# Performance work log

Hardware: AMD Instinct MI355X
Metric: run time of the kernel (lower is better)

## Reference

```python
import jax, jax.numpy as jnp
import numpy as np

B, H, S, D = 2, 16, 2048, 64
SOFTCLAMP = 50.0


def setup_inputs() -> dict:
    key = jax.random.key(0)
    kq, kk, kv, km = jax.random.split(key, 4)
    q = jax.random.normal(kq, (B, H, S, D), dtype=jnp.float32)
    k = jax.random.normal(kk, (B, H, S, D), dtype=jnp.float32)
    v = jax.random.normal(kv, (B, H, S, D), dtype=jnp.float32)
    mask = jax.random.randint(km, (B, S), 0, 2).astype(jnp.bool_)
    return {"q": q, "k": k, "v": v, "mask": mask}


def reference(q, k, v, mask):
    scale = q.shape[-1] ** -0.5
    # [b, h, i, j] similarity logits
    sim = jnp.einsum('bhid,bhjd->bhij', q, k) * scale
    # tanh-based logit softclamping (Gemma2-style softcapping)
    sim = jnp.tanh(sim / SOFTCLAMP) * SOFTCLAMP
    mask_value = -jnp.finfo(sim.dtype).max
    sim = jnp.where(mask[:, None, None, :], sim, mask_value)
    attn = jax.nn.softmax(sim, axis=-1)
    out = jnp.einsum('bhij,bhjd->bhid', attn, v)
    return out, attn
```

## Files before the change

kernel.cpp:

```cpp
#include <hip/hip_runtime.h>
#include <hip/hip_bf16.h>

#define B_ 2
#define H_ 16
#define S_ 2048
#define D_ 64
#define BUFSTR 72
#define BUFSZ (16 * BUFSTR)

typedef float f32x4 __attribute__((ext_vector_type(4)));
typedef short s16x8 __attribute__((ext_vector_type(8)));
typedef short s16x4 __attribute__((ext_vector_type(4)));

__device__ __forceinline__ short f2bf(float f) {
  unsigned u = __float_as_uint(f);
  u += 0x7FFFu + ((u >> 16) & 1u);
  return (short)(u >> 16);
}
__device__ __forceinline__ float bf2f(short s) {
  return __uint_as_float(((unsigned)(unsigned short)s) << 16);
}
__device__ __forceinline__ unsigned cvt_pk_bf16(float lo, float hi) {
  unsigned r;
  asm("v_cvt_pk_bf16_f32 %0, %1, %2" : "=v"(r) : "v"(lo), "v"(hi));
  return r;
}

__device__ __forceinline__ float softcap_p(float a) {
  const float k1 = 0.18033688011f;
  const float k2 = -3.7570183e-07f;
  const float k3 = 9.3926761e-13f;
  const float C  = 72.134752044f;
  float y = a * a;
  float t = __builtin_fmaf(y, k3, k2);
  t = __builtin_fmaf(y, t, k1);
  float arg = __builtin_fmaf(a, t, -C);
  arg = fminf(arg, 0.f);
  return exp2f(arg);
}

__global__ __launch_bounds__(256) void prep_qk(const float* __restrict__ q,
                                               const float* __restrict__ k,
                                               short* __restrict__ qbf,
                                               short* __restrict__ kbf) {
  size_t i = ((size_t)blockIdx.x * 256 + threadIdx.x) * 8;
  const f32x4* qa = (const f32x4*)(q + i);
  const f32x4* ka = (const f32x4*)(k + i);
  f32x4 a0 = __builtin_nontemporal_load(qa);
  f32x4 a1 = __builtin_nontemporal_load(qa + 1);
  f32x4 b0 = __builtin_nontemporal_load(ka);
  f32x4 b1 = __builtin_nontemporal_load(ka + 1);
  s16x8 oq, ok;
  #pragma unroll
  for (int e = 0; e < 4; ++e) {
    oq[e] = f2bf(a0[e]); oq[4 + e] = f2bf(a1[e]);
    ok[e] = f2bf(b0[e]); ok[4 + e] = f2bf(b1[e]);
  }
  *(s16x8*)(qbf + i) = oq;
  *(s16x8*)(kbf + i) = ok;
}

__global__ __launch_bounds__(256) void prep_v(const float* __restrict__ v,
                                              short* __restrict__ vt) {
  __shared__ float tile[64][65];
  const int tid = threadIdx.x;
  const int j0 = blockIdx.x * 64;
  const int bh = blockIdx.y;
  const float* vh = v + (size_t)bh * S_ * D_;
  #pragma unroll
  for (int it = 0; it < 16; ++it) {
    int idx = it * 256 + tid;
    int row = idx >> 6, col = idx & 63;
    tile[row][col] = __builtin_nontemporal_load(&vh[(size_t)(j0 + row) * D_ + col]);
  }
  __syncthreads();
  short* vth = vt + (size_t)bh * D_ * S_;
  #pragma unroll
  for (int it = 0; it < 16; ++it) {
    int idx = it * 256 + tid;
    int d = idx >> 6, jj = idx & 63;
    vth[(size_t)d * S_ + j0 + jj] = f2bf(tile[jj][d]);
  }
}

template <bool PRE>
__global__ __launch_bounds__(512, 2) void attend_fused(
    const float* __restrict__ q, const float* __restrict__ k,
    const float* __restrict__ v, const int* __restrict__ mask,
    const short* __restrict__ qbf, const short* __restrict__ kbf,
    const short* __restrict__ vt,
    float* __restrict__ out, float* __restrict__ attn) {
  __shared__ float pvred[8][16][64];
  __shared__ float ls_rs[8][16];
  __shared__ float ls_rinv[16];

  const int tid  = threadIdx.x;
  const int wv   = tid >> 6;
  const int lane = tid & 63;
  const int lg   = lane >> 4;
  const int li   = lane & 15;

  const unsigned flat = blockIdx.y * gridDim.x + blockIdx.x;
  const unsigned swz  = (flat & 7) * 512 + (flat >> 3);
  const int q0 = (int)(swz & 127) * 16;
  const int bh = (int)(swz >> 7);
  const int b  = bh >> 4;
  const int* mrow = mask + (size_t)b * S_;

  short* myb = (short*)pvred + wv * BUFSZ;

  s16x8 qf0, qf1;
  if constexpr (PRE) {
    const short* qr = qbf + ((size_t)bh * S_ + q0 + li) * D_ + lg * 8;
    qf0 = *(const s16x8*)qr;
    qf1 = *(const s16x8*)(qr + 32);
  } else {
    const float* qr = q + ((size_t)bh * S_ + q0 + li) * D_ + lg * 8;
    #pragma unroll
    for (int e = 0; e < 8; ++e) { qf0[e] = f2bf(qr[e]); qf1[e] = f2bf(qr[32 + e]); }
  }

  float rs[4] = {0.f, 0.f, 0.f, 0.f};
  f32x4 pvacc[4];
  #pragma unroll
  for (int m = 0; m < 4; ++m) pvacc[m] = (f32x4){0.f, 0.f, 0.f, 0.f};
  unsigned st[4][4][2];

  #pragma unroll
  for (int c = 0; c < 4; ++c) {
    const int jc = c * 512 + wv * 64;

    f32x4 acc[4];
    #pragma unroll
    for (int n = 0; n < 4; ++n) acc[n] = (f32x4){0.f, 0.f, 0.f, 0.f};
    #pragma unroll
    for (int n = 0; n < 4; ++n) {
      if constexpr (PRE) {
        const short* kr = kbf + ((size_t)bh * S_ + jc + n * 16 + li) * D_ + lg * 8;
        acc[n] = __builtin_amdgcn_mfma_f32_16x16x32_bf16(qf0, *(const s16x8*)kr, acc[n], 0, 0, 0);
        acc[n] = __builtin_amdgcn_mfma_f32_16x16x32_bf16(qf1, *(const s16x8*)(kr + 32), acc[n], 0, 0, 0);
      } else {
        const float* kr = k + ((size_t)bh * S_ + jc + n * 16 + li) * D_ + lg * 8;
        s16x8 k0, k1;
        #pragma unroll
        for (int e = 0; e < 8; ++e) { k0[e] = f2bf(kr[e]); k1[e] = f2bf(kr[32 + e]); }
        acc[n] = __builtin_amdgcn_mfma_f32_16x16x32_bf16(qf0, k0, acc[n], 0, 0, 0);
        acc[n] = __builtin_amdgcn_mfma_f32_16x16x32_bf16(qf1, k1, acc[n], 0, 0, 0);
      }
    }

    #pragma unroll
    for (int n = 0; n < 4; ++n) {
      const bool keep = mrow[jc + n * 16 + li] != 0;
      float p[4];
      #pragma unroll
      for (int r = 0; r < 4; ++r) {
        float pp = softcap_p(acc[n][r]);
        p[r] = keep ? pp : 0.f;
        rs[r] += p[r];
      }
      unsigned pk0 = cvt_pk_bf16(p[0], p[1]);
      unsigned pk1 = cvt_pk_bf16(p[2], p[3]);
      st[c][n][0] = pk0;
      st[c][n][1] = pk1;
      const int col = n * 16 + li;
      myb[(lg * 4 + 0) * BUFSTR + col] = (short)(pk0 & 0xFFFFu);
      myb[(lg * 4 + 1) * BUFSTR + col] = (short)(pk0 >> 16);
      myb[(lg * 4 + 2) * BUFSTR + col] = (short)(pk1 & 0xFFFFu);
      myb[(lg * 4 + 3) * BUFSTR + col] = (short)(pk1 >> 16);
    }

    #pragma unroll
    for (int ks = 0; ks < 2; ++ks) {
      s16x8 pa = *(const s16x8*)&myb[li * BUFSTR + ks * 32 + lg * 8];
      #pragma unroll
      for (int m = 0; m < 4; ++m) {
        s16x8 vb;
        if constexpr (PRE) {
          vb = *(const s16x8*)(vt + ((size_t)bh * D_ + m * 16 + li) * S_ + jc + ks * 32 + lg * 8);
        } else {
          const float* vp = v + (size_t)bh * S_ * D_ + (size_t)(jc + ks * 32 + lg * 8) * D_ + m * 16 + li;
          #pragma unroll
          for (int e = 0; e < 8; ++e) vb[e] = f2bf(vp[(size_t)e * D_]);
        }
        pvacc[m] = __builtin_amdgcn_mfma_f32_16x16x32_bf16(pa, vb, pvacc[m], 0, 0, 0);
      }
    }
  }

  #pragma unroll
  for (int r = 0; r < 4; ++r) {
    #pragma unroll
    for (int m = 1; m < 16; m <<= 1) rs[r] += __shfl_xor(rs[r], m, 64);
  }
  if (li == 0) {
    #pragma unroll
    for (int r = 0; r < 4; ++r) ls_rs[wv][lg * 4 + r] = rs[r];
  }
  __syncthreads();
  if (tid < 16) {
    float ssum = 0.f;
    #pragma unroll
    for (int w = 0; w < 8; ++w) ssum += ls_rs[w][tid];
    ls_rinv[tid] = (ssum > 0.f) ? 1.f / ssum : 0.f;
  }
  __syncthreads();

  const int rrow = lane >> 3;
  const int rseg = lane & 7;
  const float rv0 = ls_rinv[rrow];
  const float rv1 = ls_rinv[8 + rrow];
  float* abase = attn + ((size_t)bh * S_ + q0) * S_;

  #pragma unroll
  for (int c = 0; c < 4; ++c) {
    const int jc = c * 512 + wv * 64;
    #pragma unroll
    for (int n = 0; n < 4; ++n) {
      const int col = n * 16 + li;
      #pragma unroll
      for (int rr = 0; rr < 2; ++rr) {
        unsigned pk = st[c][n][rr];
        myb[(lg * 4 + 2 * rr) * BUFSTR + col] = (short)(pk & 0xFFFFu);
        myb[(lg * 4 + 2 * rr + 1) * BUFSTR + col] = (short)(pk >> 16);
      }
    }
    #pragma unroll
    for (int half = 0; half < 2; ++half) {
      const int row = half * 8 + rrow;
      const float rv = half ? rv1 : rv0;
      #pragma unroll
      for (int jh = 0; jh < 2; ++jh) {
        s16x4 pb = *(const s16x4*)&myb[row * BUFSTR + jh * 32 + rseg * 4];
        f32x4 a;
        a[0] = bf2f(pb[0]) * rv; a[1] = bf2f(pb[1]) * rv;
        a[2] = bf2f(pb[2]) * rv; a[3] = bf2f(pb[3]) * rv;
        __builtin_nontemporal_store(a, (f32x4*)(abase + (size_t)row * S_ + jc + jh * 32 + rseg * 4));
      }
    }
  }

  __syncthreads();

  #pragma unroll
  for (int m = 0; m < 4; ++m)
    #pragma unroll
    for (int r = 0; r < 4; ++r)
      pvred[wv][lg * 4 + r][m * 16 + li] = pvacc[m][r];
  __syncthreads();

  #pragma unroll
  for (int h = 0; h < 2; ++h) {
    const int idx = h * 512 + tid;
    const int qq = idx >> 6, d = idx & 63;
    float ssum = 0.f;
    #pragma unroll
    for (int w = 0; w < 8; ++w) ssum += pvred[w][qq][d];
    out[((size_t)bh * S_ + q0 + qq) * D_ + d] = ssum * ls_rinv[qq];
  }
}

extern "C" void kernel_launch(void* const* d_in, const int* in_sizes, int n_in,
                              void* d_out, int out_size, void* d_ws, size_t ws_size,
                              hipStream_t stream) {
  const float* q = (const float*)d_in[0];
  const float* k = (const float*)d_in[1];
  const float* v = (const float*)d_in[2];
  const int* mask = (const int*)d_in[3];

  float* out  = (float*)d_out;
  const size_t nel = (size_t)B_ * H_ * S_ * D_;
  float* attn = out + nel;

  dim3 grid(S_ / 16, B_ * H_);
  const size_t need = nel * 2 * 3;

  if (ws_size >= need) {
    short* qbf = (short*)d_ws;
    short* kbf = qbf + nel;
    short* vtp = kbf + nel;
    prep_qk<<<(int)(nel / (256 * 8)), 256, 0, stream>>>(q, k, qbf, kbf);
    prep_v<<<dim3(S_ / 64, B_ * H_), 256, 0, stream>>>(v, vtp);
    attend_fused<true><<<grid, 512, 0, stream>>>(q, k, v, mask, qbf, kbf, vtp, out, attn);
  } else {
    attend_fused<false><<<grid, 512, 0, stream>>>(q, k, v, mask, nullptr, nullptr, nullptr, out, attn);
  }
}
```

Measured before the change: 317.8 us.

## Keep full probability strip in LDS and prefetch next K chunk

Replaces the per-wave 16x72 bf16 scratch buffer and register-held packed probabilities with a shared 16x2056 bf16 strip covering the whole key range. Each wave then writes two complete attention rows with contiguous 1 KB-per-iteration stores instead of 64-column fragments. The QK^T K fragments are also software-prefetched one chunk ahead into registers. This raises LDS use to about 66 KB per block, which may limit the two-blocks-per-CU occupancy target, and it adds more scalar LDS stores in place of the packed conversion.

```diff
diff --git a/kernel.cpp b/kernel.cpp
--- a/kernel.cpp
+++ b/kernel.cpp
@@ -5,8 +5,7 @@
 #define H_ 16
 #define S_ 2048
 #define D_ 64
-#define BUFSTR 72
-#define BUFSZ (16 * BUFSTR)
+#define PSTR 2056
 
 typedef float f32x4 __attribute__((ext_vector_type(4)));
 typedef short s16x8 __attribute__((ext_vector_type(8)));
@@ -19,11 +18,6 @@
 }
 __device__ __forceinline__ float bf2f(short s) {
   return __uint_as_float(((unsigned)(unsigned short)s) << 16);
-}
-__device__ __forceinline__ unsigned cvt_pk_bf16(float lo, float hi) {
-  unsigned r;
-  asm("v_cvt_pk_bf16_f32 %0, %1, %2" : "=v"(r) : "v"(lo), "v"(hi));
-  return r;
 }
 
 __device__ __forceinline__ float softcap_p(float a) {
@@ -90,7 +84,7 @@
     const short* __restrict__ qbf, const short* __restrict__ kbf,
     const short* __restrict__ vt,
     float* __restrict__ out, float* __restrict__ attn) {
-  __shared__ float pvred[8][16][64];
+  __shared__ short strip[16 * PSTR];
   __shared__ float ls_rs[8][16];
   __shared__ float ls_rinv[16];
 
@@ -106,8 +100,6 @@
   const int bh = (int)(swz >> 7);
   const int b  = bh >> 4;
   const int* mrow = mask + (size_t)b * S_;
-
-  short* myb = (short*)pvred + wv * BUFSZ;
 
   s16x8 qf0, qf1;
   if constexpr (PRE) {
@@ -120,11 +112,24 @@
     for (int e = 0; e < 8; ++e) { qf0[e] = f2bf(qr[e]); qf1[e] = f2bf(qr[32 + e]); }
   }
 
+  const short* kbase = PRE ? (kbf + (size_t)bh * S_ * D_) : nullptr;
+  s16x8 kf[8];
+
+  auto ldK = [&](int cc) {
+    const int jcc = cc * 512 + wv * 64;
+    #pragma unroll
+    for (int n = 0; n < 4; ++n) {
+      const short* kr = kbase + (size_t)(jcc + n * 16 + li) * D_ + lg * 8;
+      kf[2 * n]     = *(const s16x8*)kr;
+      kf[2 * n + 1] = *(const s16x8*)(kr + 32);
+    }
+  };
+  if constexpr (PRE) ldK(0);
+
   float rs[4] = {0.f, 0.f, 0.f, 0.f};
   f32x4 pvacc[4];
   #pragma unroll
   for (int m = 0; m < 4; ++m) pvacc[m] = (f32x4){0.f, 0.f, 0.f, 0.f};
-  unsigned st[4][4][2];
 
   #pragma unroll
   for (int c = 0; c < 4; ++c) {
@@ -133,13 +138,16 @@
     f32x4 acc[4];
     #pragma unroll
     for (int n = 0; n < 4; ++n) acc[n] = (f32x4){0.f, 0.f, 0.f, 0.f};
-    #pragma unroll
-    for (int n = 0; n < 4; ++n) {
-      if constexpr (PRE) {
-        const short* kr = kbf + ((size_t)bh * S_ + jc + n * 16 + li) * D_ + lg * 8;
-        acc[n] = __builtin_amdgcn_mfma_f32_16x16x32_bf16(qf0, *(const s16x8*)kr, acc[n], 0, 0, 0);
-        acc[n] = __builtin_amdgcn_mfma_f32_16x16x32_bf16(qf1, *(const s16x8*)(kr + 32), acc[n], 0, 0, 0);
-      } else {
+    if constexpr (PRE) {
+      #pragma unroll
+      for (int n = 0; n < 4; ++n) {
+        acc[n] = __builtin_amdgcn_mfma_f32_16x16x32_bf16(qf0, kf[2 * n], acc[n], 0, 0, 0);
+        acc[n] = __builtin_amdgcn_mfma_f32_16x16x32_bf16(qf1, kf[2 * n + 1], acc[n], 0, 0, 0);
+      }
+      if (c < 3) ldK(c + 1);
+    } else {
+      #pragma unroll
+      for (int n = 0; n < 4; ++n) {
         const float* kr = k + ((size_t)bh * S_ + jc + n * 16 + li) * D_ + lg * 8;
         s16x8 k0, k1;
         #pragma unroll
@@ -151,28 +159,20 @@
 
     #pragma unroll
     for (int n = 0; n < 4; ++n) {
-      const bool keep = mrow[jc + n * 16 + li] != 0;
-      float p[4];
+      const int j = jc + n * 16 + li;
+      const bool keep = mrow[j] != 0;
       #pragma unroll
       for (int r = 0; r < 4; ++r) {
         float pp = softcap_p(acc[n][r]);
-        p[r] = keep ? pp : 0.f;
-        rs[r] += p[r];
-      }
-      unsigned pk0 = cvt_pk_bf16(p[0], p[1]);
-      unsigned pk1 = cvt_pk_bf16(p[2], p[3]);
-      st[c][n][0] = pk0;
-      st[c][n][1] = pk1;
-      const int col = n * 16 + li;
-      myb[(lg * 4 + 0) * BUFSTR + col] = (short)(pk0 & 0xFFFFu);
-      myb[(lg * 4 + 1) * BUFSTR + col] = (short)(pk0 >> 16);
-      myb[(lg * 4 + 2) * BUFSTR + col] = (short)(pk1 & 0xFFFFu);
-      myb[(lg * 4 + 3) * BUFSTR + col] = (short)(pk1 >> 16);
+        float pv_ = keep ? pp : 0.f;
+        rs[r] += pv_;
+        strip[(lg * 4 + r) * PSTR + j] = f2bf(pv_);
+      }
     }
 
     #pragma unroll
     for (int ks = 0; ks < 2; ++ks) {
-      s16x8 pa = *(const s16x8*)&myb[li * BUFSTR + ks * 32 + lg * 8];
+      s16x8 pa = *(const s16x8*)&strip[li * PSTR + jc + ks * 32 + lg * 8];
       #pragma unroll
       for (int m = 0; m < 4; ++m) {
         s16x8 vb;
@@ -206,42 +206,26 @@
   }
   __syncthreads();
 
-  const int rrow = lane >> 3;
-  const int rseg = lane & 7;
-  const float rv0 = ls_rinv[rrow];
-  const float rv1 = ls_rinv[8 + rrow];
   float* abase = attn + ((size_t)bh * S_ + q0) * S_;
-
-  #pragma unroll
-  for (int c = 0; c < 4; ++c) {
-    const int jc = c * 512 + wv * 64;
-    #pragma unroll
-    for (int n = 0; n < 4; ++n) {
-      const int col = n * 16 + li;
-      #pragma unroll
-      for (int rr = 0; rr < 2; ++rr) {
-        unsigned pk = st[c][n][rr];
-        myb[(lg * 4 + 2 * rr) * BUFSTR + col] = (short)(pk & 0xFFFFu);
-        myb[(lg * 4 + 2 * rr + 1) * BUFSTR + col] = (short)(pk >> 16);
-      }
-    }
-    #pragma unroll
-    for (int half = 0; half < 2; ++half) {
-      const int row = half * 8 + rrow;
-      const float rv = half ? rv1 : rv0;
-      #pragma unroll
-      for (int jh = 0; jh < 2; ++jh) {
-        s16x4 pb = *(const s16x4*)&myb[row * BUFSTR + jh * 32 + rseg * 4];
-        f32x4 a;
-        a[0] = bf2f(pb[0]) * rv; a[1] = bf2f(pb[1]) * rv;
-        a[2] = bf2f(pb[2]) * rv; a[3] = bf2f(pb[3]) * rv;
-        __builtin_nontemporal_store(a, (f32x4*)(abase + (size_t)row * S_ + jc + jh * 32 + rseg * 4));
-      }
-    }
-  }
-
-  __syncthreads();
-
+  #pragma unroll
+  for (int rr = 0; rr < 2; ++rr) {
+    const int row = wv * 2 + rr;
+    const float rv = ls_rinv[row];
+    const short* srow = &strip[row * PSTR];
+    float* arow = abase + (size_t)row * S_;
+    #pragma unroll
+    for (int it = 0; it < 8; ++it) {
+      s16x4 pb = *(const s16x4*)&srow[it * 256 + lane * 4];
+      f32x4 a;
+      a[0] = bf2f(pb[0]) * rv; a[1] = bf2f(pb[1]) * rv;
+      a[2] = bf2f(pb[2]) * rv; a[3] = bf2f(pb[3]) * rv;
+      __builtin_nontemporal_store(a, (f32x4*)(arow + it * 256 + lane * 4));
+    }
+  }
+
+  __syncthreads();
+
+  float (*pvred)[16][64] = (float (*)[16][64])strip;
   #pragma unroll
   for (int m = 0; m < 4; ++m)
     #pragma unroll
```

Result: faster. 309.1 us (-2.7%).
